# Optimization experiments

Measured on AMD Instinct MI355X. Metric: run time of the kernel, lower is better.

Reference implementation:

```python
import jax, jax.numpy as jnp
import numpy as np

NEG_SLOPE = 0.2

def gat_conv(x_s, x_d, src, dst, W_s, W_d, a_s, a_d, bias, n_dst):
    # PyG GATConv, heads=1, bipartite (-1,-1) input
    hs = x_s @ W_s                          # [Ns, H]
    hd = x_d @ W_d                          # [Nd, H]
    e = jnp.take(hs @ a_s, src) + jnp.take(hd @ a_d, dst)   # [E]
    e = jax.nn.leaky_relu(e, NEG_SLOPE)
    emax = jax.ops.segment_max(e, dst, num_segments=n_dst)
    emax = jax.lax.stop_gradient(jnp.where(jnp.isfinite(emax), emax, 0.0))
    w = jnp.exp(e - emax[dst])              # [E]
    den = jax.ops.segment_sum(w, dst, num_segments=n_dst)   # [Nd]
    msg = jax.ops.segment_sum(w[:, None] * hs[src], dst, num_segments=n_dst)  # [Nd, H]
    return msg / jnp.maximum(den, 1e-16)[:, None] + bias

def setup_inputs() -> dict:
    key = jax.random.key(0)
    ks = jax.random.split(key, 16)
    Na, Nw, D, H, E = 50000, 100000, 128, 128, 640000
    s = 1.0 / np.sqrt(D)
    return {
        "x_artist": jax.random.normal(ks[0], (Na, D), jnp.float32),
        "x_artwork": jax.random.normal(ks[1], (Nw, D), jnp.float32),
        "src_ca": jax.random.randint(ks[2], (E,), 0, Na, jnp.int32),
        "dst_ca": jax.random.randint(ks[3], (E,), 0, Nw, jnp.int32),
        "src_ac": jax.random.randint(ks[4], (E,), 0, Nw, jnp.int32),
        "dst_ac": jax.random.randint(ks[5], (E,), 0, Na, jnp.int32),
        "src_ww": jax.random.randint(ks[6], (E,), 0, Nw, jnp.int32),
        "dst_ww": jax.random.randint(ks[7], (E,), 0, Nw, jnp.int32),
        "Ws": jax.random.normal(ks[8], (3, D, H), jnp.float32) * s,
        "Wd": jax.random.normal(ks[9], (3, D, H), jnp.float32) * s,
        "a_s": jax.random.normal(ks[10], (3, H), jnp.float32) * s,
        "a_d": jax.random.normal(ks[11], (3, H), jnp.float32) * s,
        "b": jax.random.normal(ks[12], (3, H), jnp.float32) * 0.01,
    }

def reference(x_artist, x_artwork, src_ca, dst_ca, src_ac, dst_ac, src_ww, dst_ww, Ws, Wd, a_s, a_d, b):
    Na, Nw = x_artist.shape[0], x_artwork.shape[0]
    # edge type 0: artist->artwork (creates); 1: artwork->artist; 2: artwork->artwork
    out_aw = gat_conv(x_artist, x_artwork, src_ca, dst_ca, Ws[0], Wd[0], a_s[0], a_d[0], b[0], Nw)
    out_aw = out_aw + gat_conv(x_artwork, x_artwork, src_ww, dst_ww, Ws[2], Wd[2], a_s[2], a_d[2], b[2], Nw)  # HeteroConv aggr='sum'
    out_ar = gat_conv(x_artwork, x_artist, src_ac, dst_ac, Ws[1], Wd[1], a_s[1], a_d[1], b[1], Na)
    out_ar = jax.nn.relu(out_ar)
    out_aw = jax.nn.relu(out_aw)
    # concat node-type outputs: [Na+Nw, H]
    return jnp.concatenate([out_ar, out_aw], axis=0)
```

## Files before the change

### kernel.cpp

```cpp
#include <hip/hip_runtime.h>
#include <hip/hip_bf16.h>

#define HD 128
#define NEG_SLOPE 0.2f

typedef __attribute__((ext_vector_type(8))) short short8;
typedef __attribute__((ext_vector_type(4))) float f32x4;

__device__ __forceinline__ float lrelu(float x) {
    return x > 0.f ? x : NEG_SLOPE * x;
}
__device__ __forceinline__ ushort f2bf(float f) {
    __hip_bfloat16 h = __float2bfloat16(f);
    return *(ushort*)&h;
}
__device__ __forceinline__ float bflo(unsigned u) { return __uint_as_float(u << 16); }
__device__ __forceinline__ float bfhi(unsigned u) { return __uint_as_float(u & 0xffff0000u); }

__global__ void k_prep(const float* __restrict__ Ws, const float* __restrict__ Wd,
                       const float* __restrict__ a_s, const float* __restrict__ a_d,
                       ushort* __restrict__ Wt, ushort* __restrict__ vfA,
                       ushort* __restrict__ vfW, int* __restrict__ counts, int nTot) {
    int t = blockIdx.x * blockDim.x + threadIdx.x;
    if (t < nTot) counts[t] = 0;
    if (t < 768) {
        int c = t >> 8;
        int sd = (t >> 7) & 1;
        int d = t & (HD - 1);
        const float* W = sd ? Wd : Ws;
        const float* a = sd ? a_d : a_s;
        const float* Wrow = W + ((size_t)c * HD + d) * HD;
        const float* av = a + c * HD;
        float s = 0.f;
        for (int h = 0; h < HD; h++) s += Wrow[h] * av[h];
        ushort bs = f2bf(s);
        if (c == 0 && sd == 0)      vfA[0 * HD + d] = bs;
        else if (c == 1 && sd == 1) vfA[1 * HD + d] = bs;
        else if (c == 0 && sd == 1) vfW[0 * HD + d] = bs;
        else if (c == 1 && sd == 0) vfW[1 * HD + d] = bs;
        else if (c == 2 && sd == 0) vfW[2 * HD + d] = bs;
        else                        vfW[3 * HD + d] = bs;
    }
    int z = t - 768;
    if (z >= 0 && z < 14 * HD) vfA[2 * HD + z] = 0;
    int z2 = t - 768 - 14 * HD;
    if (z2 >= 0 && z2 < 12 * HD) vfW[4 * HD + z2] = 0;
    int u = t - 768 - 14 * HD - 12 * HD;
    if (u >= 0 && u < 3 * HD * HD) {
        int c = u >> 14;
        int r = u & 16383;
        int n = r >> 7, k = r & 127;
        Wt[u] = f2bf(Ws[((size_t)c << 14) + k * HD + n]);
    }
}

template<int NV>
__device__ __forceinline__ void gemm_body(int blk, const float* __restrict__ X,
        const ushort* __restrict__ Wt, const ushort* __restrict__ vfrag,
        ushort* __restrict__ H16,
        float* __restrict__ a0, float* __restrict__ a1,
        float* __restrict__ a2, float* __restrict__ a3, int nrows) {
    int tid = threadIdx.x;
    int lane = tid & 63;
    int wv = tid >> 6;
    int m = lane & 15;
    int kb = lane >> 4;
    long long row0 = (long long)blk * 64 + wv * 16;
    long long ar = row0 + m;
    if (ar >= nrows) ar = nrows - 1;
    const float* aptr = X + ar * HD + kb * 8;
    const ushort* bptr = Wt + (size_t)m * HD + kb * 8;

    f32x4 acc[8];
    #pragma unroll
    for (int t = 0; t < 8; t++) acc[t] = (f32x4){0.f, 0.f, 0.f, 0.f};
    f32x4 aacc = (f32x4){0.f, 0.f, 0.f, 0.f};

    #pragma unroll
    for (int ks = 0; ks < 4; ks++) {
        float4 A0 = *(const float4*)(aptr + ks * 32);
        float4 A1 = *(const float4*)(aptr + ks * 32 + 4);
        short8 af;
        af[0] = (short)f2bf(A0.x); af[1] = (short)f2bf(A0.y);
        af[2] = (short)f2bf(A0.z); af[3] = (short)f2bf(A0.w);
        af[4] = (short)f2bf(A1.x); af[5] = (short)f2bf(A1.y);
        af[6] = (short)f2bf(A1.z); af[7] = (short)f2bf(A1.w);
        #pragma unroll
        for (int t = 0; t < 8; t++) {
            short8 bf = *(const short8*)(bptr + (size_t)t * 16 * HD + ks * 32);
            acc[t] = __builtin_amdgcn_mfma_f32_16x16x32_bf16(af, bf, acc[t], 0, 0, 0);
        }
        if (NV > 0) {
            short8 vf = *(const short8*)(vfrag + (size_t)m * HD + kb * 8 + ks * 32);
            aacc = __builtin_amdgcn_mfma_f32_16x16x32_bf16(af, vf, aacc, 0, 0, 0);
        }
    }
    int rb = kb * 4;
    #pragma unroll
    for (int t = 0; t < 8; t++) {
        #pragma unroll
        for (int j = 0; j < 4; j++) {
            long long r = row0 + rb + j;
            if (r < nrows) H16[r * HD + t * 16 + m] = f2bf(acc[t][j]);
        }
    }
    if (NV > 0 && m < NV) {
        float* ao = (m == 0) ? a0 : (m == 1) ? a1 : (m == 2) ? a2 : a3;
        #pragma unroll
        for (int j = 0; j < 4; j++) {
            long long r = row0 + rb + j;
            if (r < nrows) ao[r] = aacc[j];
        }
    }
}

__global__ __launch_bounds__(256) void k_hist_gemm(
        const int* __restrict__ d0, const int* __restrict__ d1, const int* __restrict__ d2,
        int* __restrict__ counts, ushort* __restrict__ rank16, int E, int off1, int off2,
        const float* __restrict__ xa, int Na, const ushort* __restrict__ Wt0,
        const ushort* __restrict__ vfA, ushort* __restrict__ hs0,
        float* __restrict__ as0, float* __restrict__ ad1, int g0B,
        const float* __restrict__ xw, int Nw, const ushort* __restrict__ Wt2,
        const ushort* __restrict__ vfW, ushort* __restrict__ hs2,
        float* __restrict__ ad0, float* __restrict__ as1,
        float* __restrict__ as2, float* __restrict__ ad2,
        int ngemm, int total) {
    int b = blockIdx.x;
    int g0 = (int)(((long long)b * ngemm) / total);
    int g1 = (int)(((long long)(b + 1) * ngemm) / total);
    if (g1 > g0) {
        if (g0 < g0B)
            gemm_body<2>(g0, xa, Wt0, vfA, hs0, as0, ad1, nullptr, nullptr, Na);
        else
            gemm_body<4>(g0 - g0B, xw, Wt2, vfW, hs2, ad0, as1, as2, ad2, Nw);
    } else {
        int hb = b - g0;
        int t = hb * 256 + threadIdx.x;
        if (t >= 3 * E) return;
        int gd;
        if (t < E)           gd = d0[t];
        else if (t < 2 * E)  gd = off1 + d1[t - E];
        else                 gd = off2 + d2[t - 2 * E];
        rank16[t] = (ushort)atomicAdd(&counts[gd], 1);
    }
}

__global__ __launch_bounds__(256) void k_gemm1(const float* __restrict__ X,
        const ushort* __restrict__ Wt, ushort* __restrict__ H16, int nrows) {
    gemm_body<0>(blockIdx.x, X, Wt, nullptr, H16, nullptr, nullptr, nullptr, nullptr, nrows);
}

__global__ void k_chunksum(const int* __restrict__ counts, int* __restrict__ chunkSum, int n) {
    __shared__ int sh[256];
    int i = blockIdx.x * 256 + threadIdx.x;
    sh[threadIdx.x] = (i < n) ? counts[i] : 0;
    __syncthreads();
    for (int off = 128; off; off >>= 1) {
        if (threadIdx.x < off) sh[threadIdx.x] += sh[threadIdx.x + off];
        __syncthreads();
    }
    if (threadIdx.x == 0) chunkSum[blockIdx.x] = sh[0];
}

__global__ void k_scanchunk(const int* __restrict__ chunkSum, int* __restrict__ chunkOff, int nChunk) {
    __shared__ int sh[1024];
    int t = threadIdx.x;
    int v = (t < nChunk) ? chunkSum[t] : 0;
    sh[t] = v;
    __syncthreads();
    for (int off = 1; off < 1024; off <<= 1) {
        int add = (t >= off) ? sh[t - off] : 0;
        __syncthreads();
        sh[t] += add;
        __syncthreads();
    }
    if (t < nChunk) chunkOff[t] = sh[t] - v;
}

__global__ void k_rowstart(const int* __restrict__ counts, const int* __restrict__ chunkOff,
                           int* __restrict__ rowStart, int n) {
    __shared__ int sh[256];
    int i = blockIdx.x * 256 + threadIdx.x;
    int t = threadIdx.x;
    int v = (i < n) ? counts[i] : 0;
    sh[t] = v;
    __syncthreads();
    for (int off = 1; off < 256; off <<= 1) {
        int add = (t >= off) ? sh[t - off] : 0;
        __syncthreads();
        sh[t] += add;
        __syncthreads();
    }
    if (i < n) rowStart[i] = chunkOff[blockIdx.x] + sh[t] - v;
}

__global__ void k_fill3(const int* __restrict__ s0, const int* __restrict__ d0,
                        const int* __restrict__ s1, const int* __restrict__ d1,
                        const int* __restrict__ s2, const int* __restrict__ d2,
                        const float* __restrict__ as0, const float* __restrict__ as1,
                        const float* __restrict__ as2,
                        const int* __restrict__ rowStart, const ushort* __restrict__ rank16,
                        int2* __restrict__ ePair, int E, int off1, int off2) {
    int t = blockIdx.x * blockDim.x + threadIdx.x;
    if (t >= 3 * E) return;
    int sv, gd;
    const float* A;
    if (t < E)          { sv = s0[t];        gd = d0[t];        A = as0; }
    else if (t < 2 * E) { int e = t - E;     sv = s1[e]; gd = off1 + d1[e]; A = as1; }
    else                { int e = t - 2 * E; sv = s2[e]; gd = off2 + d2[e]; A = as2; }
    ePair[rowStart[gd] + rank16[t]] = make_int2(sv, __float_as_int(A[sv]));
}

__device__ __forceinline__ void seg_accum(int2 p, int dg, int base, float adv,
                                          const int2* __restrict__ ePair,
                                          const ushort* __restrict__ hs,
                                          int lane, int sub, int fl, float acc[8]) {
    if (dg <= 0) return;
    if (dg <= 64) {
        float av = (lane < dg) ? lrelu(__int_as_float(p.y) + adv) : -1e30f;
        float mm = av;
        #pragma unroll
        for (int off = 32; off; off >>= 1) mm = fmaxf(mm, __shfl_xor(mm, off, 64));
        float w = (lane < dg) ? __expf(av - mm) : 0.f;
        float den = w;
        #pragma unroll
        for (int off = 32; off; off >>= 1) den += __shfl_xor(den, off, 64);
        w *= (1.f / den);
        int s = (lane < dg) ? p.x : 0;
        for (int j0 = 0; j0 < dg; j0 += 4) {
            int idx = j0 + sub;
            float wj = __shfl(w, idx, 64);
            int sj = __shfl(s, idx, 64);
            uint4 u = *(const uint4*)((const unsigned*)hs + ((size_t)sj * HD + fl * 8) / 2);
            acc[0] += wj * bflo(u.x); acc[1] += wj * bfhi(u.x);
            acc[2] += wj * bflo(u.y); acc[3] += wj * bfhi(u.y);
            acc[4] += wj * bflo(u.z); acc[5] += wj * bfhi(u.z);
            acc[6] += wj * bflo(u.w); acc[7] += wj * bfhi(u.w);
        }
    } else {
        float mm = -1e30f;
        for (int i = lane; i < dg; i += 64) {
            int2 q = ePair[base + i];
            mm = fmaxf(mm, lrelu(__int_as_float(q.y) + adv));
        }
        #pragma unroll
        for (int off = 32; off; off >>= 1) mm = fmaxf(mm, __shfl_xor(mm, off, 64));
        float den = 0.f;
        for (int i = lane; i < dg; i += 64) {
            int2 q = ePair[base + i];
            den += __expf(lrelu(__int_as_float(q.y) + adv) - mm);
        }
        #pragma unroll
        for (int off = 32; off; off >>= 1) den += __shfl_xor(den, off, 64);
        float inv = 1.f / den;
        for (int c0 = 0; c0 < dg; c0 += 64) {
            int n = min(64, dg - c0);
            int s = 0; float w = 0.f;
            if (lane < n) {
                int2 q = ePair[base + c0 + lane];
                s = q.x;
                w = __expf(lrelu(__int_as_float(q.y) + adv) - mm) * inv;
            }
            for (int j0 = 0; j0 < n; j0 += 4) {
                int idx = j0 + sub;
                float wj = __shfl(w, idx, 64);
                int sj = __shfl(s, idx, 64);
                uint4 u = *(const uint4*)((const unsigned*)hs + ((size_t)sj * HD + fl * 8) / 2);
                acc[0] += wj * bflo(u.x); acc[1] += wj * bfhi(u.x);
                acc[2] += wj * bflo(u.y); acc[3] += wj * bfhi(u.y);
                acc[4] += wj * bflo(u.z); acc[5] += wj * bfhi(u.z);
                acc[6] += wj * bflo(u.w); acc[7] += wj * bfhi(u.w);
            }
        }
    }
}

__global__ __launch_bounds__(256) void k_agg02(const int2* __restrict__ ePair,
        const int* __restrict__ rowStart, const int* __restrict__ counts,
        const float* __restrict__ ad0_, const float* __restrict__ ad2_,
        const ushort* __restrict__ hs0, const ushort* __restrict__ hs2,
        const float* __restrict__ b0, const float* __restrict__ b2,
        float* __restrict__ out, int Nw, int offR2) {
    int lane = threadIdx.x & 63;
    int d = (int)(((long long)blockIdx.x * blockDim.x + threadIdx.x) >> 6);
    if (d >= Nw) return;
    int sub = lane >> 4, fl = lane & 15;

    int dgA = counts[d],         bA = rowStart[d];
    int dgB = counts[offR2 + d], bB = rowStart[offR2 + d];
    float aA = ad0_[d], aB = ad2_[d];
    int2 pA = make_int2(0, 0), pB = make_int2(0, 0);
    if (dgA > 0 && dgA <= 64 && lane < dgA) pA = ePair[bA + lane];
    if (dgB > 0 && dgB <= 64 && lane < dgB) pB = ePair[bB + lane];

    float acc[8];
    #pragma unroll
    for (int k = 0; k < 8; k++) acc[k] = 0.f;
    seg_accum(pA, dgA, bA, aA, ePair, hs0, lane, sub, fl, acc);
    seg_accum(pB, dgB, bB, aB, ePair, hs2, lane, sub, fl, acc);

    #pragma unroll
    for (int k = 0; k < 8; k++) {
        acc[k] += __shfl_xor(acc[k], 16, 64);
        acc[k] += __shfl_xor(acc[k], 32, 64);
    }
    if (lane < 16) {
        float* orow = out + (size_t)d * HD + fl * 8;
        float vals[8];
        #pragma unroll
        for (int k = 0; k < 8; k++)
            vals[k] = fmaxf(b0[fl * 8 + k] + b2[fl * 8 + k] + acc[k], 0.f);
        *(float4*)&orow[0] = make_float4(vals[0], vals[1], vals[2], vals[3]);
        *(float4*)&orow[4] = make_float4(vals[4], vals[5], vals[6], vals[7]);
    }
}

__global__ __launch_bounds__(256) void k_agg1(const int2* __restrict__ ePair,
        const int* __restrict__ rowStart, const int* __restrict__ counts,
        const float* __restrict__ ad_, const ushort* __restrict__ hs,
        const float* __restrict__ bias, float* __restrict__ out, int Nd) {
    int lane = threadIdx.x & 63;
    int w = (int)(((long long)blockIdx.x * blockDim.x + threadIdx.x) >> 6);
    int d0 = 2 * w, d1 = 2 * w + 1;
    if (d0 >= Nd) return;
    int sub = lane >> 4, fl = lane & 15;

    int dg0 = counts[d0], b0 = rowStart[d0];
    float a0 = ad_[d0];
    int dg1 = 0, b1 = 0; float a1 = 0.f;
    if (d1 < Nd) { dg1 = counts[d1]; b1 = rowStart[d1]; a1 = ad_[d1]; }
    int2 p0 = make_int2(0, 0), p1 = make_int2(0, 0);
    if (dg0 > 0 && dg0 <= 64 && lane < dg0) p0 = ePair[b0 + lane];
    if (dg1 > 0 && dg1 <= 64 && lane < dg1) p1 = ePair[b1 + lane];

    float acc0[8], acc1[8];
    #pragma unroll
    for (int k = 0; k < 8; k++) { acc0[k] = 0.f; acc1[k] = 0.f; }
    seg_accum(p0, dg0, b0, a0, ePair, hs, lane, sub, fl, acc0);
    seg_accum(p1, dg1, b1, a1, ePair, hs, lane, sub, fl, acc1);

    #pragma unroll
    for (int k = 0; k < 8; k++) {
        acc0[k] += __shfl_xor(acc0[k], 16, 64);
        acc0[k] += __shfl_xor(acc0[k], 32, 64);
        acc1[k] += __shfl_xor(acc1[k], 16, 64);
        acc1[k] += __shfl_xor(acc1[k], 32, 64);
    }
    if (lane < 16) {
        float* orow = out + (size_t)d0 * HD + fl * 8;
        float vals[8];
        #pragma unroll
        for (int k = 0; k < 8; k++)
            vals[k] = fmaxf(bias[fl * 8 + k] + acc0[k], 0.f);
        *(float4*)&orow[0] = make_float4(vals[0], vals[1], vals[2], vals[3]);
        *(float4*)&orow[4] = make_float4(vals[4], vals[5], vals[6], vals[7]);
        if (d1 < Nd) {
            float* orow1 = out + (size_t)d1 * HD + fl * 8;
            #pragma unroll
            for (int k = 0; k < 8; k++)
                vals[k] = fmaxf(bias[fl * 8 + k] + acc1[k], 0.f);
            *(float4*)&orow1[0] = make_float4(vals[0], vals[1], vals[2], vals[3]);
            *(float4*)&orow1[4] = make_float4(vals[4], vals[5], vals[6], vals[7]);
        }
    }
}

extern "C" void kernel_launch(void* const* d_in, const int* in_sizes, int n_in,
                              void* d_out, int out_size, void* d_ws, size_t ws_size,
                              hipStream_t stream) {
    const float* x_artist  = (const float*)d_in[0];
    const float* x_artwork = (const float*)d_in[1];
    const int* srcA[3] = {(const int*)d_in[2], (const int*)d_in[4], (const int*)d_in[6]};
    const int* dstA[3] = {(const int*)d_in[3], (const int*)d_in[5], (const int*)d_in[7]};
    const float* Ws  = (const float*)d_in[8];
    const float* Wd  = (const float*)d_in[9];
    const float* a_s = (const float*)d_in[10];
    const float* a_d = (const float*)d_in[11];
    const float* b   = (const float*)d_in[12];
    float* out = (float*)d_out;

    const int Na = in_sizes[0] / HD;
    const int Nw = in_sizes[1] / HD;
    const int E  = in_sizes[2];
    const int nTot = Nw + Na + Nw;
    const int nChunk = (nTot + 255) / 256;

    float* ws = (float*)d_ws;
    size_t off = 0;
    float* as0 = ws + off;  off += Na;
    float* ad1 = ws + off;  off += Na;
    float* ad0 = ws + off;  off += Nw;
    float* as1 = ws + off;  off += Nw;
    float* as2 = ws + off;  off += Nw;
    float* ad2 = ws + off;  off += Nw;
    int* counts   = (int*)(ws + off); off += nTot;
    int* chunkSum = (int*)(ws + off); off += 1024;
    int* chunkOff = (int*)(ws + off); off += 1024;
    int* rowStart = (int*)(ws + off); off += nTot;
    int2* ePair   = (int2*)(ws + off); off += (size_t)2 * 3 * E;
    ushort* rank16 = (ushort*)(ws + off); off += ((size_t)3 * E + 1) / 2;
    ushort* Wt    = (ushort*)(ws + off); off += (3 * HD * HD) / 2;
    ushort* vfA   = (ushort*)(ws + off); off += (16 * HD) / 2;
    ushort* vfW   = (ushort*)(ws + off); off += (16 * HD) / 2;
    ushort* hs0   = (ushort*)(ws + off); off += (size_t)Na * HD / 2;
    ushort* hs2   = (ushort*)(ws + off); off += (size_t)Nw * HD / 2;
    if (ws_size < off * sizeof(float) || nChunk > 1024) return;

    const int off1 = Nw, off2 = Nw + Na;
    const int B = 256;

    k_prep<<<(nTot + B - 1) / B, B, 0, stream>>>(Ws, Wd, a_s, a_d, Wt, vfA, vfW, counts, nTot);

    const int histB = (3 * E + B - 1) / B;
    const int g0B = (Na + 63) / 64;
    const int g2B = (Nw + 63) / 64;
    const int ngemm = g0B + g2B;
    const int total = histB + ngemm;
    k_hist_gemm<<<total, B, 0, stream>>>(dstA[0], dstA[1], dstA[2], counts, rank16,
                                         E, off1, off2,
                                         x_artist, Na, Wt + 0 * HD * HD, vfA, hs0,
                                         as0, ad1, g0B,
                                         x_artwork, Nw, Wt + 2 * HD * HD, vfW, hs2,
                                         ad0, as1, as2, ad2,
                                         ngemm, total);

    k_chunksum<<<nChunk, B, 0, stream>>>(counts, chunkSum, nTot);
    k_scanchunk<<<1, 1024, 0, stream>>>(chunkSum, chunkOff, nChunk);
    k_rowstart<<<nChunk, B, 0, stream>>>(counts, chunkOff, rowStart, nTot);

    k_fill3<<<(3 * E + B - 1) / B, B, 0, stream>>>(srcA[0], dstA[0], srcA[1], dstA[1],
                                                   srcA[2], dstA[2], as0, as1, as2,
                                                   rowStart, rank16, ePair, E, off1, off2);

    k_agg02<<<(Nw + 3) / 4, B, 0, stream>>>(ePair, rowStart, counts, ad0, ad2,
                                            hs0, hs2, b, b + 2 * HD,
                                            out + (size_t)Na * HD, Nw, off2);
    k_gemm1<<<(Nw + 63) / 64, B, 0, stream>>>(x_artwork, Wt + 1 * HD * HD, hs2, Nw);
    int nw1 = (Na + 1) / 2;
    k_agg1<<<(nw1 + 3) / 4, B, 0, stream>>>(ePair, rowStart + off1, counts + off1,
                                            ad1, hs2, b + HD, out, Na);
}
```

Baseline: 282.7 us.

## Fold artwork W1 GEMM into fused hist-GEMM launch and split GEMM into halves

When the workspace has room for another bf16 buffer, the GEMM for edge type 1's source projection moves into the combined histogram/GEMM launch and writes a separate hs1 buffer, so the standalone k_gemm1 launch after aggregation is skipped. The GEMM body now handles output columns in two halves of four tiles, and launch bounds request 8 blocks per unit, to lower register pressure and raise occupancy. The trade-off is extra workspace, and the A tile is loaded and converted twice, once per half.

```diff
diff --git a/kernel.cpp b/kernel.cpp
--- a/kernel.cpp
+++ b/kernel.cpp
@@ -60,79 +60,91 @@
         ushort* __restrict__ H16,
         float* __restrict__ a0, float* __restrict__ a1,
         float* __restrict__ a2, float* __restrict__ a3, int nrows) {
-    int tid = threadIdx.x;
-    int lane = tid & 63;
-    int wv = tid >> 6;
+    int lane = threadIdx.x & 63;
+    int wv = threadIdx.x >> 6;
     int m = lane & 15;
     int kb = lane >> 4;
     long long row0 = (long long)blk * 64 + wv * 16;
     long long ar = row0 + m;
     if (ar >= nrows) ar = nrows - 1;
     const float* aptr = X + ar * HD + kb * 8;
-    const ushort* bptr = Wt + (size_t)m * HD + kb * 8;
-
-    f32x4 acc[8];
+    const ushort* bbase = Wt + (size_t)m * HD + kb * 8;
+    int rb = kb * 4;
+
     #pragma unroll
-    for (int t = 0; t < 8; t++) acc[t] = (f32x4){0.f, 0.f, 0.f, 0.f};
-    f32x4 aacc = (f32x4){0.f, 0.f, 0.f, 0.f};
-
-    #pragma unroll
-    for (int ks = 0; ks < 4; ks++) {
-        float4 A0 = *(const float4*)(aptr + ks * 32);
-        float4 A1 = *(const float4*)(aptr + ks * 32 + 4);
-        short8 af;
-        af[0] = (short)f2bf(A0.x); af[1] = (short)f2bf(A0.y);
-        af[2] = (short)f2bf(A0.z); af[3] = (short)f2bf(A0.w);
-        af[4] = (short)f2bf(A1.x); af[5] = (short)f2bf(A1.y);
-        af[6] = (short)f2bf(A1.z); af[7] = (short)f2bf(A1.w);
-        #pragma unroll
-        for (int t = 0; t < 8; t++) {
-            short8 bf = *(const short8*)(bptr + (size_t)t * 16 * HD + ks * 32);
-            acc[t] = __builtin_amdgcn_mfma_f32_16x16x32_bf16(af, bf, acc[t], 0, 0, 0);
-        }
-        if (NV > 0) {
-            short8 vf = *(const short8*)(vfrag + (size_t)m * HD + kb * 8 + ks * 32);
-            aacc = __builtin_amdgcn_mfma_f32_16x16x32_bf16(af, vf, aacc, 0, 0, 0);
-        }
-    }
-    int rb = kb * 4;
-    #pragma unroll
-    for (int t = 0; t < 8; t++) {
-        #pragma unroll
-        for (int j = 0; j < 4; j++) {
-            long long r = row0 + rb + j;
-            if (r < nrows) H16[r * HD + t * 16 + m] = f2bf(acc[t][j]);
-        }
-    }
-    if (NV > 0 && m < NV) {
-        float* ao = (m == 0) ? a0 : (m == 1) ? a1 : (m == 2) ? a2 : a3;
-        #pragma unroll
-        for (int j = 0; j < 4; j++) {
-            long long r = row0 + rb + j;
-            if (r < nrows) ao[r] = aacc[j];
-        }
-    }
-}
-
-__global__ __launch_bounds__(256) void k_hist_gemm(
+    for (int half = 0; half < 2; half++) {
+        f32x4 acc[4];
+        #pragma unroll
+        for (int t = 0; t < 4; t++) acc[t] = (f32x4){0.f, 0.f, 0.f, 0.f};
+        f32x4 aacc = (f32x4){0.f, 0.f, 0.f, 0.f};
+
+        #pragma unroll
+        for (int ks = 0; ks < 4; ks++) {
+            float4 A0 = *(const float4*)(aptr + ks * 32);
+            float4 A1 = *(const float4*)(aptr + ks * 32 + 4);
+            short8 af;
+            af[0] = (short)f2bf(A0.x); af[1] = (short)f2bf(A0.y);
+            af[2] = (short)f2bf(A0.z); af[3] = (short)f2bf(A0.w);
+            af[4] = (short)f2bf(A1.x); af[5] = (short)f2bf(A1.y);
+            af[6] = (short)f2bf(A1.z); af[7] = (short)f2bf(A1.w);
+            #pragma unroll
+            for (int t = 0; t < 4; t++) {
+                short8 bf = *(const short8*)(bbase + (size_t)(half * 4 + t) * 16 * HD + ks * 32);
+                acc[t] = __builtin_amdgcn_mfma_f32_16x16x32_bf16(af, bf, acc[t], 0, 0, 0);
+            }
+            if (NV > 0 && half == 0) {
+                short8 vf = *(const short8*)(vfrag + (size_t)m * HD + kb * 8 + ks * 32);
+                aacc = __builtin_amdgcn_mfma_f32_16x16x32_bf16(af, vf, aacc, 0, 0, 0);
+            }
+        }
+        #pragma unroll
+        for (int t = 0; t < 4; t++) {
+            #pragma unroll
+            for (int j = 0; j < 4; j++) {
+                long long r = row0 + rb + j;
+                if (r < nrows) H16[r * HD + (half * 4 + t) * 16 + m] = f2bf(acc[t][j]);
+            }
+        }
+        if (NV > 0 && half == 0 && m < NV) {
+            float* ao = (m == 0) ? a0 : (m == 1) ? a1 : (m == 2) ? a2 : a3;
+            #pragma unroll
+            for (int j = 0; j < 4; j++) {
+                long long r = row0 + rb + j;
+                if (r < nrows) ao[r] = aacc[j];
+            }
+        }
+    }
+}
+
+__global__ __launch_bounds__(256, 8) void k_hist_gemm(
         const int* __restrict__ d0, const int* __restrict__ d1, const int* __restrict__ d2,
         int* __restrict__ counts, ushort* __restrict__ rank16, int E, int off1, int off2,
-        const float* __restrict__ xa, int Na, const ushort* __restrict__ Wt0,
-        const ushort* __restrict__ vfA, ushort* __restrict__ hs0,
-        float* __restrict__ as0, float* __restrict__ ad1, int g0B,
-        const float* __restrict__ xw, int Nw, const ushort* __restrict__ Wt2,
-        const ushort* __restrict__ vfW, ushort* __restrict__ hs2,
+        const float* __restrict__ xa, int Na, const float* __restrict__ xw, int Nw,
+        const ushort* __restrict__ Wt, const ushort* __restrict__ vfA,
+        const ushort* __restrict__ vfW,
+        ushort* __restrict__ hs0, ushort* __restrict__ hs2, ushort* __restrict__ hs1,
+        float* __restrict__ as0, float* __restrict__ ad1,
         float* __restrict__ ad0, float* __restrict__ as1,
         float* __restrict__ as2, float* __restrict__ ad2,
-        int ngemm, int total) {
+        int g0B, int g2B, int g1B, int ngemm, int total) {
     int b = blockIdx.x;
     int g0 = (int)(((long long)b * ngemm) / total);
     int g1 = (int)(((long long)(b + 1) * ngemm) / total);
     if (g1 > g0) {
-        if (g0 < g0B)
-            gemm_body<2>(g0, xa, Wt0, vfA, hs0, as0, ad1, nullptr, nullptr, Na);
-        else
-            gemm_body<4>(g0 - g0B, xw, Wt2, vfW, hs2, ad0, as1, as2, ad2, Nw);
+        if (g0 < g0B) {
+            gemm_body<2>(g0, xa, Wt, vfA, hs0, as0, ad1, nullptr, nullptr, Na);
+        } else if (g0 < g0B + g2B) {
+            int blk = g0 - g0B;
+            if (g1B > 0)
+                gemm_body<0>(blk, xw, Wt + 2 * HD * HD, nullptr, hs2,
+                             nullptr, nullptr, nullptr, nullptr, Nw);
+            else
+                gemm_body<4>(blk, xw, Wt + 2 * HD * HD, vfW, hs2,
+                             ad0, as1, as2, ad2, Nw);
+        } else {
+            gemm_body<4>(g0 - g0B - g2B, xw, Wt + 1 * HD * HD, vfW, hs1,
+                         ad0, as1, as2, ad2, Nw);
+        }
     } else {
         int hb = b - g0;
         int t = hb * 256 + threadIdx.x;
@@ -145,7 +157,7 @@
     }
 }
 
-__global__ __launch_bounds__(256) void k_gemm1(const float* __restrict__ X,
+__global__ __launch_bounds__(256, 8) void k_gemm1(const float* __restrict__ X,
         const ushort* __restrict__ Wt, ushort* __restrict__ H16, int nrows) {
     gemm_body<0>(blockIdx.x, X, Wt, nullptr, H16, nullptr, nullptr, nullptr, nullptr, nrows);
 }
@@ -406,6 +418,10 @@
     ushort* hs2   = (ushort*)(ws + off); off += (size_t)Nw * HD / 2;
     if (ws_size < off * sizeof(float) || nChunk > 1024) return;
 
+    size_t offBig = off + (size_t)Nw * HD / 2;
+    bool bigWS = (ws_size >= offBig * sizeof(float));
+    ushort* hs1 = bigWS ? (ushort*)(ws + off) : hs2;
+
     const int off1 = Nw, off2 = Nw + Na;
     const int B = 256;
 
@@ -414,15 +430,15 @@
     const int histB = (3 * E + B - 1) / B;
     const int g0B = (Na + 63) / 64;
     const int g2B = (Nw + 63) / 64;
-    const int ngemm = g0B + g2B;
+    const int g1B = bigWS ? g2B : 0;
+    const int ngemm = g0B + g2B + g1B;
     const int total = histB + ngemm;
     k_hist_gemm<<<total, B, 0, stream>>>(dstA[0], dstA[1], dstA[2], counts, rank16,
                                          E, off1, off2,
-                                         x_artist, Na, Wt + 0 * HD * HD, vfA, hs0,
-                                         as0, ad1, g0B,
-                                         x_artwork, Nw, Wt + 2 * HD * HD, vfW, hs2,
-                                         ad0, as1, as2, ad2,
-                                         ngemm, total);
+                                         x_artist, Na, x_artwork, Nw,
+                                         Wt, vfA, vfW, hs0, hs2, hs1,
+                                         as0, ad1, ad0, as1, as2, ad2,
+                                         g0B, g2B, g1B, ngemm, total);
 
     k_chunksum<<<nChunk, B, 0, stream>>>(counts, chunkSum, nTot);
     k_scanchunk<<<1, 1024, 0, stream>>>(chunkSum, chunkOff, nChunk);
@@ -435,8 +451,9 @@
     k_agg02<<<(Nw + 3) / 4, B, 0, stream>>>(ePair, rowStart, counts, ad0, ad2,
                                             hs0, hs2, b, b + 2 * HD,
                                             out + (size_t)Na * HD, Nw, off2);
-    k_gemm1<<<(Nw + 63) / 64, B, 0, stream>>>(x_artwork, Wt + 1 * HD * HD, hs2, Nw);
+    if (!bigWS)
+        k_gemm1<<<(Nw + 63) / 64, B, 0, stream>>>(x_artwork, Wt + 1 * HD * HD, hs2, Nw);
     int nw1 = (Na + 1) / 2;
     k_agg1<<<(nw1 + 3) / 4, B, 0, stream>>>(ePair, rowStart + off1, counts + off1,
-                                            ad1, hs2, b + HD, out, Na);
-}
+                                            ad1, hs1, b + HD, out, Na);
+}
```

Result: slower. 296.2 us (+4.8%).

## Fuse artwork GEMMs, merge aggregation kernels, and multi-item hist/fill threads

Applied to the files above, without the earlier changes.

Splits the combined histogram+GEMM kernel into a standalone histogram kernel that processes 8 edges per thread with batched atomics. When the workspace is large enough, the two artwork projections are computed in one GEMM kernel that shares the A-fragment loads and writes a separate hs1 buffer. That extra buffer lets all three aggregations run in a single kernel instead of agg02, a recomputing GEMM and agg1. The fill kernel now handles 4 edges per thread to increase memory-level parallelism. In exchange it needs extra workspace for hs1 and loses the previous overlap of histogram atomics with GEMM work.

```diff
diff --git a/kernel.cpp b/kernel.cpp
--- a/kernel.cpp
+++ b/kernel.cpp
@@ -60,9 +60,8 @@
         ushort* __restrict__ H16,
         float* __restrict__ a0, float* __restrict__ a1,
         float* __restrict__ a2, float* __restrict__ a3, int nrows) {
-    int tid = threadIdx.x;
-    int lane = tid & 63;
-    int wv = tid >> 6;
+    int lane = threadIdx.x & 63;
+    int wv = threadIdx.x >> 6;
     int m = lane & 15;
     int kb = lane >> 4;
     long long row0 = (long long)blk * 64 + wv * 16;
@@ -114,40 +113,117 @@
     }
 }
 
-__global__ __launch_bounds__(256) void k_hist_gemm(
-        const int* __restrict__ d0, const int* __restrict__ d1, const int* __restrict__ d2,
-        int* __restrict__ counts, ushort* __restrict__ rank16, int E, int off1, int off2,
-        const float* __restrict__ xa, int Na, const ushort* __restrict__ Wt0,
-        const ushort* __restrict__ vfA, ushort* __restrict__ hs0,
-        float* __restrict__ as0, float* __restrict__ ad1, int g0B,
-        const float* __restrict__ xw, int Nw, const ushort* __restrict__ Wt2,
-        const ushort* __restrict__ vfW, ushort* __restrict__ hs2,
-        float* __restrict__ ad0, float* __restrict__ as1,
-        float* __restrict__ as2, float* __restrict__ ad2,
-        int ngemm, int total) {
-    int b = blockIdx.x;
-    int g0 = (int)(((long long)b * ngemm) / total);
-    int g1 = (int)(((long long)(b + 1) * ngemm) / total);
-    if (g1 > g0) {
-        if (g0 < g0B)
-            gemm_body<2>(g0, xa, Wt0, vfA, hs0, as0, ad1, nullptr, nullptr, Na);
-        else
-            gemm_body<4>(g0 - g0B, xw, Wt2, vfW, hs2, ad0, as1, as2, ad2, Nw);
-    } else {
-        int hb = b - g0;
-        int t = hb * 256 + threadIdx.x;
-        if (t >= 3 * E) return;
-        int gd;
-        if (t < E)           gd = d0[t];
-        else if (t < 2 * E)  gd = off1 + d1[t - E];
-        else                 gd = off2 + d2[t - 2 * E];
-        rank16[t] = (ushort)atomicAdd(&counts[gd], 1);
-    }
-}
-
-__global__ __launch_bounds__(256) void k_gemm1(const float* __restrict__ X,
+__global__ __launch_bounds__(256) void k_gemm0(const float* __restrict__ X,
+        const ushort* __restrict__ Wt, const ushort* __restrict__ vfA,
+        ushort* __restrict__ H16, float* __restrict__ as0, float* __restrict__ ad1, int nrows) {
+    gemm_body<2>(blockIdx.x, X, Wt, vfA, H16, as0, ad1, nullptr, nullptr, nrows);
+}
+__global__ __launch_bounds__(256) void k_gemm2f(const float* __restrict__ X,
+        const ushort* __restrict__ Wt, const ushort* __restrict__ vfW,
+        ushort* __restrict__ H16, float* __restrict__ ad0, float* __restrict__ as1,
+        float* __restrict__ as2, float* __restrict__ ad2, int nrows) {
+    gemm_body<4>(blockIdx.x, X, Wt, vfW, H16, ad0, as1, as2, ad2, nrows);
+}
+__global__ __launch_bounds__(256) void k_gemm1f(const float* __restrict__ X,
         const ushort* __restrict__ Wt, ushort* __restrict__ H16, int nrows) {
     gemm_body<0>(blockIdx.x, X, Wt, nullptr, H16, nullptr, nullptr, nullptr, nullptr, nrows);
+}
+
+__global__ __launch_bounds__(256) void k_gemmW(const float* __restrict__ X,
+        const ushort* __restrict__ WtA, const ushort* __restrict__ WtB,
+        const ushort* __restrict__ vf, ushort* __restrict__ hsA, ushort* __restrict__ hsB,
+        float* __restrict__ a0, float* __restrict__ a1,
+        float* __restrict__ a2, float* __restrict__ a3, int nrows) {
+    int lane = threadIdx.x & 63;
+    int wv = threadIdx.x >> 6;
+    int m = lane & 15;
+    int kb = lane >> 4;
+    long long row0 = (long long)blockIdx.x * 64 + wv * 16;
+    long long ar = row0 + m;
+    if (ar >= nrows) ar = nrows - 1;
+    const float* aptr = X + ar * HD + kb * 8;
+    const ushort* bA = WtA + (size_t)m * HD + kb * 8;
+    const ushort* bB = WtB + (size_t)m * HD + kb * 8;
+    int rb = kb * 4;
+
+    #pragma unroll
+    for (int half = 0; half < 2; half++) {
+        f32x4 accA[4], accB[4];
+        #pragma unroll
+        for (int t = 0; t < 4; t++) {
+            accA[t] = (f32x4){0.f, 0.f, 0.f, 0.f};
+            accB[t] = (f32x4){0.f, 0.f, 0.f, 0.f};
+        }
+        f32x4 aacc = (f32x4){0.f, 0.f, 0.f, 0.f};
+        #pragma unroll
+        for (int ks = 0; ks < 4; ks++) {
+            float4 A0 = *(const float4*)(aptr + ks * 32);
+            float4 A1 = *(const float4*)(aptr + ks * 32 + 4);
+            short8 af;
+            af[0] = (short)f2bf(A0.x); af[1] = (short)f2bf(A0.y);
+            af[2] = (short)f2bf(A0.z); af[3] = (short)f2bf(A0.w);
+            af[4] = (short)f2bf(A1.x); af[5] = (short)f2bf(A1.y);
+            af[6] = (short)f2bf(A1.z); af[7] = (short)f2bf(A1.w);
+            #pragma unroll
+            for (int t = 0; t < 4; t++) {
+                short8 bfA = *(const short8*)(bA + (size_t)(half * 4 + t) * 16 * HD + ks * 32);
+                accA[t] = __builtin_amdgcn_mfma_f32_16x16x32_bf16(af, bfA, accA[t], 0, 0, 0);
+                short8 bfB = *(const short8*)(bB + (size_t)(half * 4 + t) * 16 * HD + ks * 32);
+                accB[t] = __builtin_amdgcn_mfma_f32_16x16x32_bf16(af, bfB, accB[t], 0, 0, 0);
+            }
+            if (half == 0) {
+                short8 vfr = *(const short8*)(vf + (size_t)m * HD + kb * 8 + ks * 32);
+                aacc = __builtin_amdgcn_mfma_f32_16x16x32_bf16(af, vfr, aacc, 0, 0, 0);
+            }
+        }
+        #pragma unroll
+        for (int t = 0; t < 4; t++) {
+            #pragma unroll
+            for (int j = 0; j < 4; j++) {
+                long long r = row0 + rb + j;
+                if (r < nrows) {
+                    hsA[r * HD + (half * 4 + t) * 16 + m] = f2bf(accA[t][j]);
+                    hsB[r * HD + (half * 4 + t) * 16 + m] = f2bf(accB[t][j]);
+                }
+            }
+        }
+        if (half == 0 && m < 4) {
+            float* ao = (m == 0) ? a0 : (m == 1) ? a1 : (m == 2) ? a2 : a3;
+            #pragma unroll
+            for (int j = 0; j < 4; j++) {
+                long long r = row0 + rb + j;
+                if (r < nrows) ao[r] = aacc[j];
+            }
+        }
+    }
+}
+
+__global__ __launch_bounds__(256) void k_hist3(const int* __restrict__ d0,
+        const int* __restrict__ d1, const int* __restrict__ d2,
+        int* __restrict__ counts, ushort* __restrict__ rank16,
+        int E, int off1, int off2, int S) {
+    int tid = blockIdx.x * blockDim.x + threadIdx.x;
+    int total = 3 * E;
+    int gd[8];
+    #pragma unroll
+    for (int u = 0; u < 8; u++) {
+        int t = tid + u * S;
+        gd[u] = -1;
+        if (t < total) {
+            if (t < E)          gd[u] = d0[t];
+            else if (t < 2 * E) gd[u] = off1 + d1[t - E];
+            else                gd[u] = off2 + d2[t - 2 * E];
+        }
+    }
+    int r[8];
+    #pragma unroll
+    for (int u = 0; u < 8; u++)
+        r[u] = (gd[u] >= 0) ? atomicAdd(&counts[gd[u]], 1) : 0;
+    #pragma unroll
+    for (int u = 0; u < 8; u++) {
+        int t = tid + u * S;
+        if (t < total) rank16[t] = (ushort)r[u];
+    }
 }
 
 __global__ void k_chunksum(const int* __restrict__ counts, int* __restrict__ chunkSum, int n) {
@@ -194,21 +270,39 @@
     if (i < n) rowStart[i] = chunkOff[blockIdx.x] + sh[t] - v;
 }
 
-__global__ void k_fill3(const int* __restrict__ s0, const int* __restrict__ d0,
-                        const int* __restrict__ s1, const int* __restrict__ d1,
-                        const int* __restrict__ s2, const int* __restrict__ d2,
-                        const float* __restrict__ as0, const float* __restrict__ as1,
-                        const float* __restrict__ as2,
-                        const int* __restrict__ rowStart, const ushort* __restrict__ rank16,
-                        int2* __restrict__ ePair, int E, int off1, int off2) {
-    int t = blockIdx.x * blockDim.x + threadIdx.x;
-    if (t >= 3 * E) return;
-    int sv, gd;
-    const float* A;
-    if (t < E)          { sv = s0[t];        gd = d0[t];        A = as0; }
-    else if (t < 2 * E) { int e = t - E;     sv = s1[e]; gd = off1 + d1[e]; A = as1; }
-    else                { int e = t - 2 * E; sv = s2[e]; gd = off2 + d2[e]; A = as2; }
-    ePair[rowStart[gd] + rank16[t]] = make_int2(sv, __float_as_int(A[sv]));
+__global__ __launch_bounds__(256) void k_fill3(const int* __restrict__ s0, const int* __restrict__ d0,
+        const int* __restrict__ s1, const int* __restrict__ d1,
+        const int* __restrict__ s2, const int* __restrict__ d2,
+        const float* __restrict__ as0, const float* __restrict__ as1,
+        const float* __restrict__ as2,
+        const int* __restrict__ rowStart, const ushort* __restrict__ rank16,
+        int2* __restrict__ ePair, int E, int off1, int off2, int S) {
+    int tid = blockIdx.x * blockDim.x + threadIdx.x;
+    int total = 3 * E;
+    int sv[4], gd[4];
+    const float* A[4];
+    #pragma unroll
+    for (int u = 0; u < 4; u++) {
+        int t = tid + u * S;
+        gd[u] = -1;
+        if (t < total) {
+            if (t < E)          { sv[u] = s0[t];        gd[u] = d0[t];            A[u] = as0; }
+            else if (t < 2 * E) { int e = t - E;        sv[u] = s1[e]; gd[u] = off1 + d1[e]; A[u] = as1; }
+            else                { int e = t - 2 * E;    sv[u] = s2[e]; gd[u] = off2 + d2[e]; A[u] = as2; }
+        }
+    }
+    int pos[4]; float al[4];
+    #pragma unroll
+    for (int u = 0; u < 4; u++) {
+        if (gd[u] >= 0) {
+            int t = tid + u * S;
+            pos[u] = rowStart[gd[u]] + rank16[t];
+            al[u] = A[u][sv[u]];
+        }
+    }
+    #pragma unroll
+    for (int u = 0; u < 4; u++)
+        if (gd[u] >= 0) ePair[pos[u]] = make_int2(sv[u], __float_as_int(al[u]));
 }
 
 __device__ __forceinline__ void seg_accum(int2 p, int dg, int base, float adv,
@@ -275,70 +369,58 @@
     }
 }
 
-__global__ __launch_bounds__(256) void k_agg02(const int2* __restrict__ ePair,
+__device__ __forceinline__ void agg02_wave(int d, int lane, const int2* __restrict__ ePair,
         const int* __restrict__ rowStart, const int* __restrict__ counts,
         const float* __restrict__ ad0_, const float* __restrict__ ad2_,
         const ushort* __restrict__ hs0, const ushort* __restrict__ hs2,
-        const float* __restrict__ b0, const float* __restrict__ b2,
-        float* __restrict__ out, int Nw, int offR2) {
-    int lane = threadIdx.x & 63;
-    int d = (int)(((long long)blockIdx.x * blockDim.x + threadIdx.x) >> 6);
-    if (d >= Nw) return;
+        const float* __restrict__ b, float* __restrict__ out, int Na, int offR2) {
     int sub = lane >> 4, fl = lane & 15;
-
     int dgA = counts[d],         bA = rowStart[d];
     int dgB = counts[offR2 + d], bB = rowStart[offR2 + d];
     float aA = ad0_[d], aB = ad2_[d];
     int2 pA = make_int2(0, 0), pB = make_int2(0, 0);
     if (dgA > 0 && dgA <= 64 && lane < dgA) pA = ePair[bA + lane];
     if (dgB > 0 && dgB <= 64 && lane < dgB) pB = ePair[bB + lane];
-
     float acc[8];
     #pragma unroll
     for (int k = 0; k < 8; k++) acc[k] = 0.f;
     seg_accum(pA, dgA, bA, aA, ePair, hs0, lane, sub, fl, acc);
     seg_accum(pB, dgB, bB, aB, ePair, hs2, lane, sub, fl, acc);
-
     #pragma unroll
     for (int k = 0; k < 8; k++) {
         acc[k] += __shfl_xor(acc[k], 16, 64);
         acc[k] += __shfl_xor(acc[k], 32, 64);
     }
     if (lane < 16) {
-        float* orow = out + (size_t)d * HD + fl * 8;
+        float* orow = out + ((size_t)Na + d) * HD + fl * 8;
         float vals[8];
         #pragma unroll
         for (int k = 0; k < 8; k++)
-            vals[k] = fmaxf(b0[fl * 8 + k] + b2[fl * 8 + k] + acc[k], 0.f);
+            vals[k] = fmaxf(b[fl * 8 + k] + b[2 * HD + fl * 8 + k] + acc[k], 0.f);
         *(float4*)&orow[0] = make_float4(vals[0], vals[1], vals[2], vals[3]);
         *(float4*)&orow[4] = make_float4(vals[4], vals[5], vals[6], vals[7]);
     }
 }
 
-__global__ __launch_bounds__(256) void k_agg1(const int2* __restrict__ ePair,
-        const int* __restrict__ rowStart, const int* __restrict__ counts,
-        const float* __restrict__ ad_, const ushort* __restrict__ hs,
-        const float* __restrict__ bias, float* __restrict__ out, int Nd) {
-    int lane = threadIdx.x & 63;
-    int w = (int)(((long long)blockIdx.x * blockDim.x + threadIdx.x) >> 6);
-    int d0 = 2 * w, d1 = 2 * w + 1;
-    if (d0 >= Nd) return;
+__device__ __forceinline__ void agg1_wave(int ww, int lane, const int2* __restrict__ ePair,
+        const int* __restrict__ rowStart1, const int* __restrict__ counts1,
+        const float* __restrict__ ad1_, const ushort* __restrict__ hs1,
+        const float* __restrict__ bias, float* __restrict__ out, int Na) {
     int sub = lane >> 4, fl = lane & 15;
-
-    int dg0 = counts[d0], b0 = rowStart[d0];
-    float a0 = ad_[d0];
+    int d0 = 2 * ww, d1 = d0 + 1;
+    if (d0 >= Na) return;
+    int dg0 = counts1[d0], b0 = rowStart1[d0];
+    float a0 = ad1_[d0];
     int dg1 = 0, b1 = 0; float a1 = 0.f;
-    if (d1 < Nd) { dg1 = counts[d1]; b1 = rowStart[d1]; a1 = ad_[d1]; }
+    if (d1 < Na) { dg1 = counts1[d1]; b1 = rowStart1[d1]; a1 = ad1_[d1]; }
     int2 p0 = make_int2(0, 0), p1 = make_int2(0, 0);
     if (dg0 > 0 && dg0 <= 64 && lane < dg0) p0 = ePair[b0 + lane];
     if (dg1 > 0 && dg1 <= 64 && lane < dg1) p1 = ePair[b1 + lane];
-
     float acc0[8], acc1[8];
     #pragma unroll
     for (int k = 0; k < 8; k++) { acc0[k] = 0.f; acc1[k] = 0.f; }
-    seg_accum(p0, dg0, b0, a0, ePair, hs, lane, sub, fl, acc0);
-    seg_accum(p1, dg1, b1, a1, ePair, hs, lane, sub, fl, acc1);
-
+    seg_accum(p0, dg0, b0, a0, ePair, hs1, lane, sub, fl, acc0);
+    seg_accum(p1, dg1, b1, a1, ePair, hs1, lane, sub, fl, acc1);
     #pragma unroll
     for (int k = 0; k < 8; k++) {
         acc0[k] += __shfl_xor(acc0[k], 16, 64);
@@ -354,7 +436,7 @@
             vals[k] = fmaxf(bias[fl * 8 + k] + acc0[k], 0.f);
         *(float4*)&orow[0] = make_float4(vals[0], vals[1], vals[2], vals[3]);
         *(float4*)&orow[4] = make_float4(vals[4], vals[5], vals[6], vals[7]);
-        if (d1 < Nd) {
+        if (d1 < Na) {
             float* orow1 = out + (size_t)d1 * HD + fl * 8;
             #pragma unroll
             for (int k = 0; k < 8; k++)
@@ -363,6 +445,43 @@
             *(float4*)&orow1[4] = make_float4(vals[4], vals[5], vals[6], vals[7]);
         }
     }
+}
+
+__global__ __launch_bounds__(256) void k_aggAll(const int2* __restrict__ ePair,
+        const int* __restrict__ rowStart, const int* __restrict__ counts,
+        const float* __restrict__ ad0_, const float* __restrict__ ad2_,
+        const float* __restrict__ ad1_,
+        const ushort* __restrict__ hs0, const ushort* __restrict__ hs2,
+        const ushort* __restrict__ hs1,
+        const float* __restrict__ b, float* __restrict__ out,
+        int Na, int Nw, int off1, int off2) {
+    int lane = threadIdx.x & 63;
+    int w = (int)(((long long)blockIdx.x * blockDim.x + threadIdx.x) >> 6);
+    if (w < Nw) {
+        agg02_wave(w, lane, ePair, rowStart, counts, ad0_, ad2_, hs0, hs2, b, out, Na, off2);
+    } else {
+        agg1_wave(w - Nw, lane, ePair, rowStart + off1, counts + off1, ad1_, hs1,
+                  b + HD, out, Na);
+    }
+}
+
+__global__ __launch_bounds__(256) void k_agg02(const int2* __restrict__ ePair,
+        const int* __restrict__ rowStart, const int* __restrict__ counts,
+        const float* __restrict__ ad0_, const float* __restrict__ ad2_,
+        const ushort* __restrict__ hs0, const ushort* __restrict__ hs2,
+        const float* __restrict__ b, float* __restrict__ out, int Na, int Nw, int offR2) {
+    int lane = threadIdx.x & 63;
+    int d = (int)(((long long)blockIdx.x * blockDim.x + threadIdx.x) >> 6);
+    if (d < Nw)
+        agg02_wave(d, lane, ePair, rowStart, counts, ad0_, ad2_, hs0, hs2, b, out, Na, offR2);
+}
+__global__ __launch_bounds__(256) void k_agg1(const int2* __restrict__ ePair,
+        const int* __restrict__ rowStart1, const int* __restrict__ counts1,
+        const float* __restrict__ ad1_, const ushort* __restrict__ hs1,
+        const float* __restrict__ bias, float* __restrict__ out, int Na) {
+    int lane = threadIdx.x & 63;
+    int w = (int)(((long long)blockIdx.x * blockDim.x + threadIdx.x) >> 6);
+    agg1_wave(w, lane, ePair, rowStart1, counts1, ad1_, hs1, bias, out, Na);
 }
 
 extern "C" void kernel_launch(void* const* d_in, const int* in_sizes, int n_in,
@@ -406,37 +525,60 @@
     ushort* hs2   = (ushort*)(ws + off); off += (size_t)Nw * HD / 2;
     if (ws_size < off * sizeof(float) || nChunk > 1024) return;
 
+    size_t offBig = off + (size_t)Nw * HD / 2;
+    bool bigWS = (ws_size >= offBig * sizeof(float));
+    ushort* hs1 = bigWS ? (ushort*)(ws + off) : hs2;
+
     const int off1 = Nw, off2 = Nw + Na;
     const int B = 256;
+    const int total = 3 * E;
 
     k_prep<<<(nTot + B - 1) / B, B, 0, stream>>>(Ws, Wd, a_s, a_d, Wt, vfA, vfW, counts, nTot);
 
-    const int histB = (3 * E + B - 1) / B;
-    const int g0B = (Na + 63) / 64;
-    const int g2B = (Nw + 63) / 64;
-    const int ngemm = g0B + g2B;
-    const int total = histB + ngemm;
-    k_hist_gemm<<<total, B, 0, stream>>>(dstA[0], dstA[1], dstA[2], counts, rank16,
-                                         E, off1, off2,
-                                         x_artist, Na, Wt + 0 * HD * HD, vfA, hs0,
-                                         as0, ad1, g0B,
-                                         x_artwork, Nw, Wt + 2 * HD * HD, vfW, hs2,
-                                         ad0, as1, as2, ad2,
-                                         ngemm, total);
+    {
+        int nthr = (total + 7) / 8;
+        int blocks = (nthr + B - 1) / B;
+        int S = blocks * B;
+        k_hist3<<<blocks, B, 0, stream>>>(dstA[0], dstA[1], dstA[2], counts, rank16,
+                                          E, off1, off2, S);
+    }
 
     k_chunksum<<<nChunk, B, 0, stream>>>(counts, chunkSum, nTot);
     k_scanchunk<<<1, 1024, 0, stream>>>(chunkSum, chunkOff, nChunk);
     k_rowstart<<<nChunk, B, 0, stream>>>(counts, chunkOff, rowStart, nTot);
 
-    k_fill3<<<(3 * E + B - 1) / B, B, 0, stream>>>(srcA[0], dstA[0], srcA[1], dstA[1],
-                                                   srcA[2], dstA[2], as0, as1, as2,
-                                                   rowStart, rank16, ePair, E, off1, off2);
-
-    k_agg02<<<(Nw + 3) / 4, B, 0, stream>>>(ePair, rowStart, counts, ad0, ad2,
-                                            hs0, hs2, b, b + 2 * HD,
-                                            out + (size_t)Na * HD, Nw, off2);
-    k_gemm1<<<(Nw + 63) / 64, B, 0, stream>>>(x_artwork, Wt + 1 * HD * HD, hs2, Nw);
-    int nw1 = (Na + 1) / 2;
-    k_agg1<<<(nw1 + 3) / 4, B, 0, stream>>>(ePair, rowStart + off1, counts + off1,
-                                            ad1, hs2, b + HD, out, Na);
-}
+    k_gemm0<<<(Na + 63) / 64, B, 0, stream>>>(x_artist, Wt + 0 * HD * HD, vfA,
+                                              hs0, as0, ad1, Na);
+    if (bigWS) {
+        k_gemmW<<<(Nw + 63) / 64, B, 0, stream>>>(x_artwork, Wt + 1 * HD * HD,
+                                                  Wt + 2 * HD * HD, vfW, hs1, hs2,
+                                                  ad0, as1, as2, ad2, Nw);
+    } else {
+        k_gemm2f<<<(Nw + 63) / 64, B, 0, stream>>>(x_artwork, Wt + 2 * HD * HD, vfW,
+                                                   hs2, ad0, as1, as2, ad2, Nw);
+    }
+
+    {
+        int nthr = (total + 3) / 4;
+        int blocks = (nthr + B - 1) / B;
+        int S = blocks * B;
+        k_fill3<<<blocks, B, 0, stream>>>(srcA[0], dstA[0], srcA[1], dstA[1],
+                                          srcA[2], dstA[2], as0, as1, as2,
+                                          rowStart, rank16, ePair, E, off1, off2, S);
+    }
+
+    if (bigWS) {
+        int nw1 = (Na + 1) / 2;
+        long long totalW = (long long)Nw + nw1;
+        k_aggAll<<<(unsigned)((totalW + 3) / 4), B, 0, stream>>>(
+            ePair, rowStart, counts, ad0, ad2, ad1, hs0, hs2, hs1,
+            b, out, Na, Nw, off1, off2);
+    } else {
+        k_agg02<<<(Nw + 3) / 4, B, 0, stream>>>(ePair, rowStart, counts, ad0, ad2,
+                                                hs0, hs2, b, out, Na, Nw, off2);
+        k_gemm1f<<<(Nw + 63) / 64, B, 0, stream>>>(x_artwork, Wt + 1 * HD * HD, hs2, Nw);
+        int nw1 = (Na + 1) / 2;
+        k_agg1<<<(nw1 + 3) / 4, B, 0, stream>>>(ePair, rowStart + off1, counts + off1,
+                                                ad1, hs2, b + HD, out, Na);
+    }
+}
```

After: 329.1 us. 1.16x slower.
